# Performance work log

Hardware: AMD Instinct MI355X
Metric: run time of the kernel (lower is better)

## Reference

```python
import jax, jax.numpy as jnp
import numpy as np


def conv1x1(x, w, b):
    # x: [B,C,H,W], w: [O,C], b: [O]
    return jnp.einsum('bchw,oc->bohw', x, w) + b[None, :, None, None]


def dwconv(x, w):
    # depthwise conv, x: [B,C,H,W], w: [C,1,k,k], SAME padding (k odd, pad=k//2)
    return jax.lax.conv_general_dilated(
        x, w, window_strides=(1, 1), padding='SAME',
        dimension_numbers=('NCHW', 'OIHW', 'NCHW'),
        feature_group_count=x.shape[1])


def setup_inputs() -> dict:
    key = jax.random.key(0)
    ks = jax.random.split(key, 14)
    B, C, H, W = 16, 256, 64, 64
    OC = C // 16  # scale=16 -> 16
    WSCALE = 0.05
    r = lambda k, shape: jax.random.normal(k, shape, dtype=jnp.float32) * WSCALE
    return {
        'x': jax.random.normal(ks[0], (B, C, H, W), dtype=jnp.float32),
        'conv_w': r(ks[1], (C + 4, C)),           # 1x1 conv -> ctx (C) + gates (3+1)
        'conv_b': r(ks[2], (C + 4,)),
        'fw3': r(ks[3], (C, 1, 3, 3)),            # depthwise focal kernels
        'fw5': r(ks[4], (C, 1, 5, 5)),
        'fw7': r(ks[5], (C, 1, 7, 7)),
        'key_w': r(ks[6], (1, C)),                # Conv_key 1x1
        'key_b': r(ks[7], (1,)),
        'v1_w': r(ks[8], (OC, C)),                # Conv_value first 1x1
        'v1_b': r(ks[9], (OC,)),
        'ln_w': jnp.ones((OC,), dtype=jnp.float32),
        'ln_b': jnp.zeros((OC,), dtype=jnp.float32),
        'v2_w': r(ks[10], (C, OC)),               # Conv_value second 1x1
        'v2_b': r(ks[11], (C,)),
    }


def reference(x, conv_w, conv_b, fw3, fw5, fw7, key_w, key_b,
              v1_w, v1_b, ln_w, ln_b, v2_w, v2_b):
    B, C, H, W = x.shape
    # _contextAggregation
    t = conv1x1(x, conv_w, conv_b)          # [B, C+4, H, W]
    ctx, gates = t[:, :C], t[:, C:]         # [B,C,H,W], [B,4,H,W]
    ctx_all = jnp.zeros_like(ctx)
    for l, fw in enumerate((fw3, fw5, fw7)):
        ctx = jax.nn.gelu(dwconv(ctx, fw), approximate=False)  # torch GELU = exact erf
        ctx_all = ctx_all + ctx * gates[:, l:l + 1]
    ctx_global = jnp.mean(ctx, axis=(2, 3), keepdims=True)     # AdaptiveAvgPool2d(1)
    ctx_all = ctx_all + ctx_global * gates[:, 3:4]
    # GC-style channel attention: softmax over spatial positions
    k = conv1x1(ctx_all, key_w, key_b).reshape(B, H * W)       # [B, HW]
    k = jax.nn.softmax(k, axis=1)
    q = ctx_all.reshape(B, C, H * W)
    qk = jnp.einsum('bcn,bn->bc', q, k)[:, :, None, None]      # [B,C,1,1]
    # Conv_value: 1x1 -> LayerNorm([OC,1,1]) -> ReLU -> 1x1
    v = conv1x1(qk, v1_w, v1_b)                                # [B,OC,1,1]
    mu = jnp.mean(v, axis=(1, 2, 3), keepdims=True)
    var = jnp.var(v, axis=(1, 2, 3), keepdims=True)
    v = (v - mu) * jax.lax.rsqrt(var + 1e-5)
    v = v * ln_w[None, :, None, None] + ln_b[None, :, None, None]
    v = jax.nn.relu(v)
    v = conv1x1(v, v2_w, v2_b)                                 # [B,C,1,1]
    return ctx_all + v
```

## Files before the change

### kernel.cpp

```cpp
#include <hip/hip_runtime.h>

#define DEVFN __device__ __forceinline__

constexpr int B  = 16;
constexpr int C  = 256;
constexpr int N  = 64 * 64;
constexpr int O1 = C + 4;

typedef __attribute__((ext_vector_type(8)))  short bf16x8;
typedef __attribute__((ext_vector_type(4)))  short bf16x4;
typedef __attribute__((ext_vector_type(16))) float f32x16;
typedef __attribute__((ext_vector_type(2)))  _Float16 h2;
typedef unsigned short ushort_t;
typedef unsigned int   uint32;

DEVFN short f2bf(float f){
  union { float f; unsigned u; } p; p.f = f;
  unsigned r = p.u + 0x7fffu + ((p.u >> 16) & 1u);
  return (short)(r >> 16);
}
DEVFN unsigned pack2(float lo, float hi){
  return (unsigned)(ushort_t)f2bf(lo) | ((unsigned)(ushort_t)f2bf(hi) << 16);
}
DEVFN float lo2f(unsigned u){ union{unsigned u; float f;} p; p.u = u << 16; return p.f; }
DEVFN float hi2f(unsigned u){ union{unsigned u; float f;} p; p.u = u & 0xffff0000u; return p.f; }
DEVFN float bf2f(ushort_t s){ union{unsigned u; float f;} p; p.u = (unsigned)s << 16; return p.f; }

DEVFN float gelu_fast(float x){
  float s = x * x;
  float t = x * fmaf(s, 0.1029432f, 2.3022082f);
  float e = __builtin_amdgcn_exp2f(-t);
  return x * __builtin_amdgcn_rcpf(1.0f + e);
}

DEVFN float fdot2f(uint32 a, uint32 b, float c){
#if __has_builtin(__builtin_amdgcn_fdot2)
  return __builtin_amdgcn_fdot2(__builtin_bit_cast(h2, a),
                                __builtin_bit_cast(h2, b), c, false);
#else
  h2 ha = __builtin_bit_cast(h2, a), hb = __builtin_bit_cast(h2, b);
  return fmaf((float)ha.x, (float)hb.x, fmaf((float)ha.y, (float)hb.y, c));
#endif
}

DEVFN uint32 pkh(float a, float b){
  _Float16 ha = (_Float16)a, hb = (_Float16)b;
  return (uint32)__builtin_bit_cast(ushort_t, ha) |
         ((uint32)__builtin_bit_cast(ushort_t, hb) << 16);
}

__global__ __launch_bounds__(256)
void k_wbf(const float* __restrict__ w, ushort_t* __restrict__ wbf,
           const float* __restrict__ fw3, const float* __restrict__ fw5,
           const float* __restrict__ fw7, uint32* __restrict__ w3p,
           uint32* __restrict__ w5p, uint32* __restrict__ w7p){
  if(blockIdx.x == 320){
    const int c = threadIdx.x;
    #pragma unroll
    for(int ky = 0; ky < 3; ky++){
      const float* wr = fw3 + c * 9 + ky * 3;
      w3p[c * 6 + ky * 2 + 0] = pkh(wr[0], wr[1]);
      w3p[c * 6 + ky * 2 + 1] = pkh(wr[2], 0.f);
    }
    #pragma unroll
    for(int ky = 0; ky < 5; ky++){
      const float* wr = fw5 + c * 25 + ky * 5;
      w5p[c * 15 + ky * 3 + 0] = pkh(wr[0], wr[1]);
      w5p[c * 15 + ky * 3 + 1] = pkh(wr[2], wr[3]);
      w5p[c * 15 + ky * 3 + 2] = pkh(wr[4], 0.f);
    }
    #pragma unroll
    for(int ky = 0; ky < 7; ky++){
      const float* wr = fw7 + c * 49 + ky * 7;
      w7p[c * 28 + ky * 4 + 0] = pkh(wr[0], wr[1]);
      w7p[c * 28 + ky * 4 + 1] = pkh(wr[2], wr[3]);
      w7p[c * 28 + ky * 4 + 2] = pkh(wr[4], wr[5]);
      w7p[c * 28 + ky * 4 + 3] = pkh(wr[6], 0.f);
    }
    return;
  }
  int idx = blockIdx.x * 256 + threadIdx.x;
  int o = idx >> 8, cc = idx & 255;
  wbf[idx] = (o < O1) ? (ushort_t)f2bf(w[o * 256 + cc]) : (ushort_t)0;
}

__global__ __launch_bounds__(512, 6)
void k_conv1_mfma(const float* __restrict__ x, const ushort_t* __restrict__ wbf,
                  const float* __restrict__ conv_w, const float* __restrict__ bias,
                  ushort_t* __restrict__ ctxb, float* __restrict__ gates){
  __shared__ __align__(16) short wlds[8 * 256 * 8];
  __shared__ __align__(16) short xlds[8 * 64 * 8];
  __shared__ float sgw[4 * 256];
  __shared__ float sbias[256];
  const int tid  = threadIdx.x;
  const int wave = tid >> 6;
  const int lane = tid & 63;
  const int l31  = lane & 31;
  const int lhi  = lane >> 5;
  const int pg   = blockIdx.x;
  const int b    = pg >> 6;
  const int n0   = (pg & 63) * 64;

  #pragma unroll
  for(int i = 0; i < 2; i++) sgw[i * 512 + tid] = conv_w[256 * 256 + i * 512 + tid];
  if(tid < 256) sbias[tid] = bias[tid];
  const int gidx = tid >> 6;
  const int gn   = tid & 63;
  float gbias = (tid < 256) ? bias[256 + gidx] : 0.f;
  float gacc = 0.f;

  const float* xpb = x + (size_t)b * C * N + n0;

  f32x16 acc[2];
  #pragma unroll
  for(int t = 0; t < 2; t++)
    #pragma unroll
    for(int r = 0; r < 16; r++) acc[t][r] = 0.f;

  float xf[8];

  auto pfX = [&](int kc){
    const int kg = wave, n = lane;
    const float* xp = xpb + (size_t)(kc + kg * 8) * N + n;
    #pragma unroll
    for(int j = 0; j < 8; j++) xf[j] = xp[(size_t)j * N];
  };
  auto stX = [&](){
    const int kg = wave, n = lane;
    uint4 v;
    v.x = pack2(xf[0], xf[1]); v.y = pack2(xf[2], xf[3]);
    v.z = pack2(xf[4], xf[5]); v.w = pack2(xf[6], xf[7]);
    *(uint4*)&xlds[(kg * 64 + n) * 8] = v;
  };
  auto glW = [&](int kc){
    #pragma unroll
    for(int q = 0; q < 4; q++){
      const int pidx = q * 512 + tid;
      const int kg = pidx >> 8;
      const int m  = pidx & 255;
      const ushort_t* src = wbf + (size_t)m * 256 + kc + kg * 8;
      __builtin_amdgcn_global_load_lds(
          (const __attribute__((address_space(1))) unsigned int*)src,
          (__attribute__((address_space(3))) unsigned int*)&wlds[(size_t)pidx * 8],
          16, 0, 0);
    }
  };
  auto mfmaC = [&](){
    #pragma unroll
    for(int ks = 0; ks < 4; ks++){
      const int kg = ks * 2 + lhi;
      bf16x8 af = *(const bf16x8*)&wlds[(kg * 256 + wave * 32 + l31) * 8];
      bf16x8 b0 = *(const bf16x8*)&xlds[(kg * 64 + l31) * 8];
      bf16x8 b1 = *(const bf16x8*)&xlds[(kg * 64 + 32 + l31) * 8];
      acc[0] = __builtin_amdgcn_mfma_f32_32x32x16_bf16(af, b0, acc[0], 0, 0, 0);
      acc[1] = __builtin_amdgcn_mfma_f32_32x32x16_bf16(af, b1, acc[1], 0, 0, 0);
    }
  };
  auto gateC = [&](int kc){
    if(tid < 256){
      float a = gacc;
      #pragma unroll
      for(int kg = 0; kg < 8; kg++){
        bf16x8 xv = *(const bf16x8*)&xlds[(kg * 64 + gn) * 8];
        const float* gw = &sgw[gidx * 256 + kc + kg * 8];
        #pragma unroll
        for(int j = 0; j < 4; j++){
          unsigned u = ((const unsigned*)&xv)[j];
          a = fmaf(lo2f(u), gw[2 * j], a);
          a = fmaf(hi2f(u), gw[2 * j + 1], a);
        }
      }
      gacc = a;
    }
  };

  glW(0); pfX(0); stX();
  __syncthreads();
  pfX(64);
  mfmaC(); gateC(0);
  __syncthreads();
  glW(64); stX();
  __syncthreads();
  pfX(128);
  mfmaC(); gateC(64);
  __syncthreads();
  glW(128); stX();
  __syncthreads();
  pfX(192);
  mfmaC(); gateC(128);
  __syncthreads();
  glW(192); stX();
  __syncthreads();
  mfmaC(); gateC(192);

  #pragma unroll
  for(int nt = 0; nt < 2; nt++){
    const int n = n0 + nt * 32 + l31;
    #pragma unroll
    for(int r = 0; r < 16; r++){
      const int row = (r & 3) + 8 * (r >> 2) + 4 * lhi;
      const int o = wave * 32 + row;
      const float v = acc[nt][r] + sbias[o];
      _Float16 hv = (_Float16)v;
      ctxb[((size_t)(b * 256 + o)) * N + n] = __builtin_bit_cast(ushort_t, hv);
    }
  }
  if(tid < 256)
    gates[((size_t)(b * 4 + gidx)) * N + n0 + gn] = gacc + gbias;
}

constexpr int SSTR = 72;

template<int K>
DEVFN void dw_stage_dot(const short* src, const uint32* __restrict__ wp,
                        int h, int w0, float* val){
  constexpr int R = K / 2;
  constexpr int PAIRS = (K + 2) / 2;
  float acc[8];
  #pragma unroll
  for(int i = 0; i < 8; i++) acc[i] = 0.f;
  #pragma unroll
  for(int ky = 0; ky < K; ky++){
    uint32 wk[PAIRS];
    #pragma unroll
    for(int t = 0; t < PAIRS; t++) wk[t] = wp[ky * PAIRS + t];
    const int r = h + ky - R;
    if((unsigned)r < 64u){
      const short* rp = &src[r * SSTR + w0];
      uint4 a0 = *(const uint4*)rp;
      uint4 a1 = *(const uint4*)(rp + 8);
      uint32 P[8] = {a0.x, a0.y, a0.z, a0.w, a1.x, a1.y, a1.z, a1.w};
      uint32 S[7];
      #pragma unroll
      for(int j = 0; j < 7; j++)
        S[j] = __builtin_amdgcn_alignbit(P[j + 1], P[j], 16);
      #pragma unroll
      for(int i = 0; i < 8; i++){
        int j0, useP;
        if      (K == 7){ useP =  (i & 1); j0 = (i + 1) >> 1; }
        else if (K == 5){ useP = !(i & 1); j0 = (i >> 1) + 1; }
        else            { useP =  (i & 1); j0 = (i >> 1) + ((i & 1) ? 2 : 1); }
        #pragma unroll
        for(int t = 0; t < PAIRS; t++){
          const uint32 a = useP ? P[j0 + t] : S[j0 + t];
          acc[i] = fdot2f(a, wk[t], acc[i]);
        }
      }
    }
  }
  #pragma unroll
  for(int i = 0; i < 8; i++) val[i] = gelu_fast(acc[i]);
}

DEVFN void store_row_h(short* dst, int h, int w0, const float* val){
  uint32 o0 = __builtin_bit_cast(uint32, __builtin_amdgcn_cvt_pkrtz(val[0], val[1]));
  uint32 o1 = __builtin_bit_cast(uint32, __builtin_amdgcn_cvt_pkrtz(val[2], val[3]));
  uint32 o2 = __builtin_bit_cast(uint32, __builtin_amdgcn_cvt_pkrtz(val[4], val[5]));
  uint32 o3 = __builtin_bit_cast(uint32, __builtin_amdgcn_cvt_pkrtz(val[6], val[7]));
  uint2 t0; t0.x = o0; t0.y = o1;
  uint2 t1; t1.x = o2; t1.y = o3;
  *(uint2*)&dst[h * SSTR + w0 + 4] = t0;
  *(uint2*)&dst[h * SSTR + w0 + 8] = t1;
}

__global__ __launch_bounds__(512, 8)
void k_dwchain(ushort_t* __restrict__ ctxb, const uint32* __restrict__ w3p,
               const uint32* __restrict__ w5p, const uint32* __restrict__ w7p,
               const float* __restrict__ gates){
  __shared__ __align__(16) short bufA[64 * SSTR];
  __shared__ __align__(16) short bufB[64 * SSTR];
  __shared__ float wred[8];
  const int tid = threadIdx.x;
  const int plane = blockIdx.x;
  const int b = plane >> 8;
  const int c = plane & 255;
  const int h  = tid >> 3;
  const int w0 = (tid & 7) * 8;
  const int nbase = h * 64 + w0;

  if(tid < 64){
    bf16x4 z = {0, 0, 0, 0};
    *(bf16x4*)&bufA[tid * SSTR] = z;  *(bf16x4*)&bufA[tid * SSTR + 68] = z;
    *(bf16x4*)&bufB[tid * SSTR] = z;  *(bf16x4*)&bufB[tid * SSTR + 68] = z;
  }
  {
    const uint4 iv = *(const uint4*)((const short*)ctxb + (size_t)plane * N + tid * 8);
    uint2 t0; t0.x = iv.x; t0.y = iv.y;
    uint2 t1; t1.x = iv.z; t1.y = iv.w;
    *(uint2*)&bufA[h * SSTR + w0 + 4] = t0;
    *(uint2*)&bufA[h * SSTR + w0 + 8] = t1;
  }
  __syncthreads();

  float ctxp[8];
  #pragma unroll
  for(int i = 0; i < 8; i++) ctxp[i] = 0.f;
  float val[8];

  dw_stage_dot<3>(bufA, w3p + c * 6, h, w0, val);
  {
    const float* gp = gates + ((size_t)(b * 4 + 0)) * N + nbase;
    float4 ga = *(const float4*)gp, gb = *(const float4*)(gp + 4);
    ctxp[0] = fmaf(val[0], ga.x, ctxp[0]); ctxp[1] = fmaf(val[1], ga.y, ctxp[1]);
    ctxp[2] = fmaf(val[2], ga.z, ctxp[2]); ctxp[3] = fmaf(val[3], ga.w, ctxp[3]);
    ctxp[4] = fmaf(val[4], gb.x, ctxp[4]); ctxp[5] = fmaf(val[5], gb.y, ctxp[5]);
    ctxp[6] = fmaf(val[6], gb.z, ctxp[6]); ctxp[7] = fmaf(val[7], gb.w, ctxp[7]);
    store_row_h(bufB, h, w0, val);
  }
  __syncthreads();

  dw_stage_dot<5>(bufB, w5p + c * 15, h, w0, val);
  {
    const float* gp = gates + ((size_t)(b * 4 + 1)) * N + nbase;
    float4 ga = *(const float4*)gp, gb = *(const float4*)(gp + 4);
    ctxp[0] = fmaf(val[0], ga.x, ctxp[0]); ctxp[1] = fmaf(val[1], ga.y, ctxp[1]);
    ctxp[2] = fmaf(val[2], ga.z, ctxp[2]); ctxp[3] = fmaf(val[3], ga.w, ctxp[3]);
    ctxp[4] = fmaf(val[4], gb.x, ctxp[4]); ctxp[5] = fmaf(val[5], gb.y, ctxp[5]);
    ctxp[6] = fmaf(val[6], gb.z, ctxp[6]); ctxp[7] = fmaf(val[7], gb.w, ctxp[7]);
    store_row_h(bufA, h, w0, val);
  }
  __syncthreads();

  dw_stage_dot<7>(bufA, w7p + c * 28, h, w0, val);
  float lsum = 0.f;
  {
    const float* gp = gates + ((size_t)(b * 4 + 2)) * N + nbase;
    float4 ga = *(const float4*)gp, gb = *(const float4*)(gp + 4);
    ctxp[0] = fmaf(val[0], ga.x, ctxp[0]); ctxp[1] = fmaf(val[1], ga.y, ctxp[1]);
    ctxp[2] = fmaf(val[2], ga.z, ctxp[2]); ctxp[3] = fmaf(val[3], ga.w, ctxp[3]);
    ctxp[4] = fmaf(val[4], gb.x, ctxp[4]); ctxp[5] = fmaf(val[5], gb.y, ctxp[5]);
    ctxp[6] = fmaf(val[6], gb.z, ctxp[6]); ctxp[7] = fmaf(val[7], gb.w, ctxp[7]);
    #pragma unroll
    for(int i = 0; i < 8; i++) lsum += val[i];
  }
  #pragma unroll
  for(int off = 32; off > 0; off >>= 1) lsum += __shfl_xor(lsum, off, 64);
  if((tid & 63) == 0) wred[tid >> 6] = lsum;
  __syncthreads();
  float mean = 0.f;
  #pragma unroll
  for(int i = 0; i < 8; i++) mean += wred[i];
  mean *= (1.0f / 4096.0f);

  {
    const float* gp = gates + ((size_t)(b * 4 + 3)) * N + nbase;
    float4 ga = *(const float4*)gp, gb = *(const float4*)(gp + 4);
    bf16x8 ov;
    ov[0] = f2bf(fmaf(mean, ga.x, ctxp[0])); ov[1] = f2bf(fmaf(mean, ga.y, ctxp[1]));
    ov[2] = f2bf(fmaf(mean, ga.z, ctxp[2])); ov[3] = f2bf(fmaf(mean, ga.w, ctxp[3]));
    ov[4] = f2bf(fmaf(mean, gb.x, ctxp[4])); ov[5] = f2bf(fmaf(mean, gb.y, ctxp[5]));
    ov[6] = f2bf(fmaf(mean, gb.z, ctxp[6])); ov[7] = f2bf(fmaf(mean, gb.w, ctxp[7]));
    *(bf16x8*)((short*)ctxb + (size_t)plane * N + nbase) = ov;
  }
}

__global__ __launch_bounds__(256)
void k_logits(const ushort_t* __restrict__ P, const float* __restrict__ key_w,
              const float* __restrict__ key_b, float* __restrict__ logits){
  __shared__ float kw[256];
  __shared__ float part[512];
  int tid = threadIdx.x;
  kw[tid] = key_w[tid];
  __syncthreads();
  int b  = blockIdx.x >> 5;
  int n0 = (blockIdx.x & 31) * 128;
  int cpart = tid >> 6, pxp = tid & 63;
  const ushort_t* pp = P + ((size_t)(b * 256 + cpart * 64)) * N + n0 + pxp * 2;
  float a0 = 0.f, a1 = 0.f;
  #pragma unroll 8
  for(int c = 0; c < 64; c++){
    unsigned u = *(const unsigned*)(pp + (size_t)c * N);
    float kwv = kw[cpart * 64 + c];
    a0 = fmaf(lo2f(u), kwv, a0);
    a1 = fmaf(hi2f(u), kwv, a1);
  }
  part[cpart * 128 + pxp * 2]     = a0;
  part[cpart * 128 + pxp * 2 + 1] = a1;
  __syncthreads();
  if(tid < 128){
    float l = part[tid] + part[128 + tid] + part[256 + tid] + part[384 + tid];
    logits[b * N + n0 + tid] = l + key_b[0];
  }
}

__global__ __launch_bounds__(1024)
void k_softmax(float* __restrict__ kbuf){
  __shared__ float wred[16];
  int b = blockIdx.x, tid = threadIdx.x;
  const int wave = tid >> 6, lane = tid & 63;
  float v[4];
  float m = -1e30f;
  #pragma unroll
  for(int i = 0; i < 4; i++){
    v[i] = kbuf[b * N + tid + i * 1024];
    m = fmaxf(m, v[i]);
  }
  #pragma unroll
  for(int off = 32; off > 0; off >>= 1) m = fmaxf(m, __shfl_xor(m, off, 64));
  if(lane == 0) wred[wave] = m;
  __syncthreads();
  float mm = -1e30f;
  #pragma unroll
  for(int i = 0; i < 16; i++) mm = fmaxf(mm, wred[i]);
  __syncthreads();
  float s = 0.f;
  #pragma unroll
  for(int i = 0; i < 4; i++){ v[i] = __expf(v[i] - mm); s += v[i]; }
  #pragma unroll
  for(int off = 32; off > 0; off >>= 1) s += __shfl_xor(s, off, 64);
  if(lane == 0) wred[wave] = s;
  __syncthreads();
  float tot = 0.f;
  #pragma unroll
  for(int i = 0; i < 16; i++) tot += wred[i];
  float inv = 1.0f / tot;
  #pragma unroll
  for(int i = 0; i < 4; i++)
    kbuf[b * N + tid + i * 1024] = v[i] * inv;
}

__global__ __launch_bounds__(256)
void k_qk(const ushort_t* __restrict__ P, const float* __restrict__ kbuf,
          float* __restrict__ qk){
  __shared__ float red[256];
  int plane = blockIdx.x, tid = threadIdx.x;
  int b = plane >> 8;
  const unsigned* pp = (const unsigned*)(P + (size_t)plane * N);
  const float2* kp = (const float2*)(kbuf + b * N);
  float acc = 0.f;
  #pragma unroll
  for(int i = 0; i < 8; i++){
    int idx = tid + i * 256;
    unsigned u = pp[idx];
    float2 kk = kp[idx];
    acc = fmaf(lo2f(u), kk.x, acc);
    acc = fmaf(hi2f(u), kk.y, acc);
  }
  red[tid] = acc; __syncthreads();
  for(int s = 128; s > 0; s >>= 1){
    if(tid < s) red[tid] += red[tid + s];
    __syncthreads();
  }
  if(tid == 0) qk[plane] = red[0];
}

__global__ __launch_bounds__(256)
void k_v(const float* __restrict__ qk, const float* __restrict__ v1w,
         const float* __restrict__ v1b, const float* __restrict__ lnw,
         const float* __restrict__ lnb, const float* __restrict__ v2w,
         const float* __restrict__ v2b, float* __restrict__ vout){
  int b = blockIdx.x, tid = threadIdx.x;
  __shared__ float qs[256];
  __shared__ float part[256];
  __shared__ float v1s[16];
  __shared__ float vr[16];
  __shared__ float stats[2];
  qs[tid] = qk[b * 256 + tid];
  __syncthreads();
  int oc = tid >> 4, ln = tid & 15;
  float p = 0.f;
  #pragma unroll
  for(int j = 0; j < 16; j++){
    int cc = ln + j * 16;
    p = fmaf(v1w[oc * 256 + cc], qs[cc], p);
  }
  part[tid] = p;
  __syncthreads();
  if(tid < 16){
    float s = v1b[tid];
    for(int j = 0; j < 16; j++) s += part[tid * 16 + j];
    v1s[tid] = s;
  }
  __syncthreads();
  if(tid == 0){
    float mu = 0.f;
    for(int i = 0; i < 16; i++) mu += v1s[i];
    mu *= (1.f / 16.f);
    float var = 0.f;
    for(int i = 0; i < 16; i++){ float d = v1s[i] - mu; var += d * d; }
    var *= (1.f / 16.f);
    stats[0] = mu; stats[1] = rsqrtf(var + 1e-5f);
  }
  __syncthreads();
  if(tid < 16){
    float vv = (v1s[tid] - stats[0]) * stats[1] * lnw[tid] + lnb[tid];
    vr[tid] = fmaxf(vv, 0.f);
  }
  __syncthreads();
  float o = v2b[tid];
  #pragma unroll
  for(int j = 0; j < 16; j++) o = fmaf(v2w[tid * 16 + j], vr[j], o);
  vout[b * 256 + tid] = o;
}

__global__ __launch_bounds__(256)
void k_final(float* __restrict__ out, const ushort_t* __restrict__ ctxb,
             const float* __restrict__ vout){
  int idx8 = blockIdx.x * 256 + threadIdx.x;
  int plane = idx8 >> 9;
  int off = (idx8 & 511) * 8;
  bf16x8 v = *(const bf16x8*)((const short*)ctxb + (size_t)plane * N + off);
  float vv = vout[plane];
  float4 o0, o1;
  o0.x = bf2f((ushort_t)v[0]) + vv; o0.y = bf2f((ushort_t)v[1]) + vv;
  o0.z = bf2f((ushort_t)v[2]) + vv; o0.w = bf2f((ushort_t)v[3]) + vv;
  o1.x = bf2f((ushort_t)v[4]) + vv; o1.y = bf2f((ushort_t)v[5]) + vv;
  o1.z = bf2f((ushort_t)v[6]) + vv; o1.w = bf2f((ushort_t)v[7]) + vv;
  float* op = out + (size_t)plane * N + off;
  *(float4*)op = o0;
  *(float4*)(op + 4) = o1;
}

extern "C" void kernel_launch(void* const* d_in, const int* in_sizes, int n_in,
                              void* d_out, int out_size, void* d_ws, size_t ws_size,
                              hipStream_t stream){
  const float* x      = (const float*)d_in[0];
  const float* conv_w = (const float*)d_in[1];
  const float* conv_b = (const float*)d_in[2];
  const float* fw3    = (const float*)d_in[3];
  const float* fw5    = (const float*)d_in[4];
  const float* fw7    = (const float*)d_in[5];
  const float* key_w  = (const float*)d_in[6];
  const float* key_b  = (const float*)d_in[7];
  const float* v1_w   = (const float*)d_in[8];
  const float* v1_b   = (const float*)d_in[9];
  const float* ln_w   = (const float*)d_in[10];
  const float* ln_b   = (const float*)d_in[11];
  const float* v2_w   = (const float*)d_in[12];
  const float* v2_b   = (const float*)d_in[13];
  float* out = (float*)d_out;

  const size_t PL = (size_t)B * C * N;
  char* p = (char*)d_ws;
  ushort_t* ctxb = (ushort_t*)p;  p += PL * sizeof(ushort_t);
  float* gates   = (float*)p;     p += (size_t)B * 4 * N * sizeof(float);
  float* kbuf    = (float*)p;     p += (size_t)B * N * sizeof(float);
  float* qkb     = (float*)p;     p += (size_t)B * C * sizeof(float);
  float* vout    = (float*)p;     p += (size_t)B * C * sizeof(float);
  ushort_t* wbf  = (ushort_t*)p;  p += (size_t)320 * 256 * sizeof(ushort_t);
  uint32* w3p    = (uint32*)p;    p += (size_t)256 * 6 * sizeof(uint32);
  uint32* w5p    = (uint32*)p;    p += (size_t)256 * 15 * sizeof(uint32);
  uint32* w7p    = (uint32*)p;

  k_wbf<<<321, 256, 0, stream>>>(conv_w, wbf, fw3, fw5, fw7, w3p, w5p, w7p);
  k_conv1_mfma<<<1024, 512, 0, stream>>>(x, wbf, conv_w, conv_b, ctxb, gates);
  k_dwchain<<<B * C, 512, 0, stream>>>(ctxb, w3p, w5p, w7p, gates);
  k_logits<<<512, 256, 0, stream>>>(ctxb, key_w, key_b, kbuf);
  k_softmax<<<B, 1024, 0, stream>>>(kbuf);
  k_qk<<<B * C, 256, 0, stream>>>(ctxb, kbuf, qkb);
  k_v<<<B, 256, 0, stream>>>(qkb, v1_w, v1_b, ln_w, ln_b, v2_w, v2_b, vout);
  k_final<<<8192, 256, 0, stream>>>(out, ctxb, vout);
}
```

Before: 283.6 us.

## Pre-pack x to bf16 channel-interleaved layout and stream via async LDS loads

Adds a pre-pass in the weight-conversion kernel that converts x from fp32 NCHW into a bf16 layout grouping 8 channels per position, stored temporarily in the output buffer. The 1x1-conv MFMA kernel then loads x tiles straight into double-buffered LDS with global_load_lds instead of loading fp32 through registers, packing and storing them. This removes register staging and conversion from the GEMM's critical path and lets loads overlap compute. The cost is an extra full pass that reads x and writes a half-size copy, plus reuse of the output buffer as scratch.

After: 266.8 us. 5.9% less time.

```diff
diff --git a/kernel.cpp b/kernel.cpp
--- a/kernel.cpp
+++ b/kernel.cpp
@@ -53,7 +53,32 @@
 void k_wbf(const float* __restrict__ w, ushort_t* __restrict__ wbf,
            const float* __restrict__ fw3, const float* __restrict__ fw5,
            const float* __restrict__ fw7, uint32* __restrict__ w3p,
-           uint32* __restrict__ w5p, uint32* __restrict__ w7p){
+           uint32* __restrict__ w5p, uint32* __restrict__ w7p,
+           const float* __restrict__ x, ushort_t* __restrict__ xbf){
+  if(blockIdx.x >= 321){
+    const int blk = blockIdx.x - 321;
+    const int b  = blk >> 5;
+    const int kg = blk & 31;
+    const float* xs = x + ((size_t)(b * 256 + kg * 8)) * N;
+    ushort_t* xd = xbf + ((size_t)(b * 32 + kg)) * N * 8;
+    #pragma unroll
+    for(int it = 0; it < 4; it++){
+      const int n = (it * 256 + threadIdx.x) * 4;
+      float4 cv[8];
+      #pragma unroll
+      for(int j = 0; j < 8; j++) cv[j] = *(const float4*)(xs + (size_t)j * N + n);
+      #pragma unroll
+      for(int p = 0; p < 4; p++){
+        uint4 v;
+        v.x = pack2(((const float*)&cv[0])[p], ((const float*)&cv[1])[p]);
+        v.y = pack2(((const float*)&cv[2])[p], ((const float*)&cv[3])[p]);
+        v.z = pack2(((const float*)&cv[4])[p], ((const float*)&cv[5])[p]);
+        v.w = pack2(((const float*)&cv[6])[p], ((const float*)&cv[7])[p]);
+        *(uint4*)(xd + (size_t)(n + p) * 8) = v;
+      }
+    }
+    return;
+  }
   if(blockIdx.x == 320){
     const int c = threadIdx.x;
     #pragma unroll
@@ -85,11 +110,11 @@
 }
 
 __global__ __launch_bounds__(512, 6)
-void k_conv1_mfma(const float* __restrict__ x, const ushort_t* __restrict__ wbf,
+void k_conv1_mfma(const ushort_t* __restrict__ xbf, const ushort_t* __restrict__ wbf,
                   const float* __restrict__ conv_w, const float* __restrict__ bias,
                   ushort_t* __restrict__ ctxb, float* __restrict__ gates){
   __shared__ __align__(16) short wlds[8 * 256 * 8];
-  __shared__ __align__(16) short xlds[8 * 64 * 8];
+  __shared__ __align__(16) short xlds[2][8 * 64 * 8];
   __shared__ float sgw[4 * 256];
   __shared__ float sbias[256];
   const int tid  = threadIdx.x;
@@ -109,28 +134,18 @@
   float gbias = (tid < 256) ? bias[256 + gidx] : 0.f;
   float gacc = 0.f;
 
-  const float* xpb = x + (size_t)b * C * N + n0;
-
   f32x16 acc[2];
   #pragma unroll
   for(int t = 0; t < 2; t++)
     #pragma unroll
     for(int r = 0; r < 16; r++) acc[t][r] = 0.f;
 
-  float xf[8];
-
-  auto pfX = [&](int kc){
-    const int kg = wave, n = lane;
-    const float* xp = xpb + (size_t)(kc + kg * 8) * N + n;
-    #pragma unroll
-    for(int j = 0; j < 8; j++) xf[j] = xp[(size_t)j * N];
-  };
-  auto stX = [&](){
-    const int kg = wave, n = lane;
-    uint4 v;
-    v.x = pack2(xf[0], xf[1]); v.y = pack2(xf[2], xf[3]);
-    v.z = pack2(xf[4], xf[5]); v.w = pack2(xf[6], xf[7]);
-    *(uint4*)&xlds[(kg * 64 + n) * 8] = v;
+  auto glX = [&](int kc, int bf){
+    const ushort_t* src = xbf + ((size_t)(b * 32 + (kc >> 3) + wave) * N + n0 + lane) * 8;
+    __builtin_amdgcn_global_load_lds(
+        (const __attribute__((address_space(1))) unsigned int*)src,
+        (__attribute__((address_space(3))) unsigned int*)&xlds[bf][(size_t)tid * 8],
+        16, 0, 0);
   };
   auto glW = [&](int kc){
     #pragma unroll
@@ -145,23 +160,23 @@
           16, 0, 0);
     }
   };
-  auto mfmaC = [&](){
+  auto mfmaC = [&](const short* xb){
     #pragma unroll
     for(int ks = 0; ks < 4; ks++){
       const int kg = ks * 2 + lhi;
       bf16x8 af = *(const bf16x8*)&wlds[(kg * 256 + wave * 32 + l31) * 8];
-      bf16x8 b0 = *(const bf16x8*)&xlds[(kg * 64 + l31) * 8];
-      bf16x8 b1 = *(const bf16x8*)&xlds[(kg * 64 + 32 + l31) * 8];
+      bf16x8 b0 = *(const bf16x8*)&xb[(kg * 64 + l31) * 8];
+      bf16x8 b1 = *(const bf16x8*)&xb[(kg * 64 + 32 + l31) * 8];
       acc[0] = __builtin_amdgcn_mfma_f32_32x32x16_bf16(af, b0, acc[0], 0, 0, 0);
       acc[1] = __builtin_amdgcn_mfma_f32_32x32x16_bf16(af, b1, acc[1], 0, 0, 0);
     }
   };
-  auto gateC = [&](int kc){
+  auto gateC = [&](const short* xb, int kc){
     if(tid < 256){
       float a = gacc;
       #pragma unroll
       for(int kg = 0; kg < 8; kg++){
-        bf16x8 xv = *(const bf16x8*)&xlds[(kg * 64 + gn) * 8];
+        bf16x8 xv = *(const bf16x8*)&xb[(kg * 64 + gn) * 8];
         const float* gw = &sgw[gidx * 256 + kc + kg * 8];
         #pragma unroll
         for(int j = 0; j < 4; j++){
@@ -174,24 +189,24 @@
     }
   };
 
-  glW(0); pfX(0); stX();
-  __syncthreads();
-  pfX(64);
-  mfmaC(); gateC(0);
-  __syncthreads();
-  glW(64); stX();
-  __syncthreads();
-  pfX(128);
-  mfmaC(); gateC(64);
-  __syncthreads();
-  glW(128); stX();
-  __syncthreads();
-  pfX(192);
-  mfmaC(); gateC(128);
-  __syncthreads();
-  glW(192); stX();
-  __syncthreads();
-  mfmaC(); gateC(192);
+  glX(0, 0); glW(0);
+  __syncthreads();
+  glX(64, 1);
+  mfmaC(xlds[0]); gateC(xlds[0], 0);
+  __syncthreads();
+  glW(64);
+  __syncthreads();
+  glX(128, 0);
+  mfmaC(xlds[1]); gateC(xlds[1], 64);
+  __syncthreads();
+  glW(128);
+  __syncthreads();
+  glX(192, 1);
+  mfmaC(xlds[0]); gateC(xlds[0], 128);
+  __syncthreads();
+  glW(192);
+  __syncthreads();
+  mfmaC(xlds[1]); gateC(xlds[1], 192);
 
   #pragma unroll
   for(int nt = 0; nt < 2; nt++){
@@ -541,9 +556,11 @@
   uint32* w3p    = (uint32*)p;    p += (size_t)256 * 6 * sizeof(uint32);
   uint32* w5p    = (uint32*)p;    p += (size_t)256 * 15 * sizeof(uint32);
   uint32* w7p    = (uint32*)p;
-
-  k_wbf<<<321, 256, 0, stream>>>(conv_w, wbf, fw3, fw5, fw7, w3p, w5p, w7p);
-  k_conv1_mfma<<<1024, 512, 0, stream>>>(x, wbf, conv_w, conv_b, ctxb, gates);
+  ushort_t* xbf  = (ushort_t*)d_out;
+
+  k_wbf<<<833, 256, 0, stream>>>(conv_w, wbf, fw3, fw5, fw7, w3p, w5p, w7p,
+                                 x, xbf);
+  k_conv1_mfma<<<1024, 512, 0, stream>>>(xbf, wbf, conv_w, conv_b, ctxb, gates);
   k_dwchain<<<B * C, 512, 0, stream>>>(ctxb, w3p, w5p, w7p, gates);
   k_logits<<<512, 256, 0, stream>>>(ctxb, key_w, key_b, kbuf);
   k_softmax<<<B, 1024, 0, stream>>>(kbuf);
```
